# Kernel tuning notes

Hardware: AMD Instinct MI355X
Metric: run time of the kernel (lower is better)

Reference implementation:

```python
import jax, jax.numpy as jnp
import numpy as np

B, T, E, H = 64, 26, 300, 1024
FEAT, C = 2048, 7
S = C * C                  # 49 spatial positions
MCBD = 5000                # MCB_output_dim
D1 = MCBD * S              # mcb1 sketch dim = 245000
D2 = MCBD                  # mcb2 sketch dim
MCB_OUT, FACTOR = 1000, 5
VOCAB = 3000
EPS = 1e-12


def _count_sketch(x, h, s, d):
    # x: (B, n), h: (n,) int32 in [0, d), s: (n,) +-1 float -> (B, d)
    return jnp.zeros((x.shape[0], d), x.dtype).at[:, h].add(x * s)


def _cbp(x, y, hx, sx, hy, sy, d):
    # Compact bilinear pooling: count sketch both inputs, convolve via FFT.
    fx = jnp.fft.rfft(_count_sketch(x, hx, sx, d), n=d, axis=-1)
    fy = jnp.fft.rfft(_count_sketch(y, hy, sy, d), n=d, axis=-1)
    return jnp.fft.irfft(fx * fy, n=d, axis=-1)


def _lstm(x, W_ih, W_hh, b_ih, b_hh):
    # x: (T, B, E) -> hs: (T, B, H); torch gate order i, f, g, o
    xW = jnp.einsum('tbe,ge->tbg', x, W_ih) + b_ih + b_hh
    h0 = jnp.zeros((x.shape[1], W_hh.shape[1]), x.dtype)
    def step(carry, xt):
        h, c = carry
        g = xt + h @ W_hh.T
        i, f, gg, o = jnp.split(g, 4, axis=-1)
        c = jax.nn.sigmoid(f) * c + jax.nn.sigmoid(i) * jnp.tanh(gg)
        h = jax.nn.sigmoid(o) * jnp.tanh(c)
        return (h, c), h
    _, hs = jax.lax.scan(step, (h0, h0), xW)
    return hs


def _signed_sqrt(x):
    # sqrt(relu(x)) - sqrt(relu(-x)) == sign(x) * sqrt(|x|)
    return jnp.sign(x) * jnp.sqrt(jnp.abs(x))


def _l2norm(x):
    # F.normalize(x, dim=1)
    return x / jnp.maximum(jnp.linalg.norm(x, axis=1, keepdims=True), EPS)


def setup_inputs():
    key = jax.random.key(0)
    ks = jax.random.split(key, 32)
    f = lambda k, shp, sc=1.0: jax.random.normal(k, shp, jnp.float32) * sc
    ri = lambda k, shp, mx: jax.random.randint(k, shp, 0, mx, jnp.int32)
    return {
        'ques_embed': f(ks[0], (B, T, E)),
        'img_feat': f(ks[1], (B, C, C, FEAT)),
        'W_ih': f(ks[2], (4 * H, E), 0.02),
        'W_hh': f(ks[3], (4 * H, H), 0.02),
        'b_ih': f(ks[4], (4 * H,), 0.02),
        'b_hh': f(ks[5], (4 * H,), 0.02),
        'Wq1': f(ks[6], (512, H), 0.02),
        'bq1': f(ks[7], (512,), 0.02),
        'Wq2': f(ks[8], (2, 512), 0.02),
        'bq2': f(ks[9], (2,), 0.02),
        'Wi1': f(ks[10], (512, MCB_OUT), 0.02),
        'bi1': f(ks[11], (512,), 0.02),
        'Wi2': f(ks[12], (2, 512), 0.02),
        'bi2': f(ks[13], (2,), 0.02),
        'Wp': f(ks[14], (VOCAB, MCB_OUT), 0.02),
        'bp': f(ks[15], (VOCAB,), 0.02),
        'h1x': ri(ks[16], (FEAT * S,), D1),
        's1x': ri(ks[17], (FEAT * S,), 2),
        'h1q': ri(ks[18], (2 * H,), D1),
        's1q': ri(ks[19], (2 * H,), 2),
        'h2i': ri(ks[20], (2 * FEAT,), D2),
        's2i': ri(ks[21], (2 * FEAT,), 2),
        'h2q': ri(ks[22], (2 * H,), D2),
        's2q': ri(ks[23], (2 * H,), 2),
    }


def reference(ques_embed, img_feat, W_ih, W_hh, b_ih, b_hh, Wq1, bq1, Wq2, bq2,
              Wi1, bi1, Wi2, bi2, Wp, bp,
              h1x, s1x, h1q, s1q, h2i, s2i, h2q, s2q):
    sgn = lambda s: (2 * s - 1).astype(jnp.float32)
    img = jnp.transpose(img_feat, (0, 3, 1, 2)).reshape(B, FEAT, S)  # (B, feat, S)
    hs = _lstm(jnp.transpose(ques_embed, (1, 0, 2)), W_ih, W_hh, b_ih, b_hh)
    lstm1 = jnp.transpose(hs, (1, 2, 0))  # (B, H, T)
    # --- question attention (1x1 convs over (H, T)) ---
    qa = jax.nn.relu(jnp.einsum('oh,bht->bot', Wq1, lstm1) + bq1[None, :, None])
    qa = jnp.einsum('go,bot->bgt', Wq2, qa) + bq2[None, :, None]
    qatt = jax.nn.softmax(qa, axis=-1)  # (B, 2, T)
    q_feat = jnp.einsum('bgt,bht->bgh', qatt, lstm1).reshape(B, 2 * H)  # (B, 2048)
    # --- image attention with MCB1 ---
    iq = _cbp(img.reshape(B, FEAT * S), q_feat, h1x, sgn(s1x), h1q, sgn(s1q), D1)
    # (B, 5000*S) -> view (B,5000,S) -> split 5000 into (1000,5), sum factor -> (B,1000,S)
    iq = iq.reshape(B, MCB_OUT, FACTOR, S).sum(axis=2)
    iq = _l2norm(_signed_sqrt(iq).reshape(B, MCB_OUT * S)).reshape(B, MCB_OUT, S)
    ia = jax.nn.relu(jnp.einsum('om,bms->bos', Wi1, iq) + bi1[None, :, None])
    ia = jnp.einsum('go,bos->bgs', Wi2, ia) + bi2[None, :, None]
    iatt = jax.nn.softmax(ia, axis=-1)  # (B, 2, S)
    i_feat = jnp.einsum('bgs,bfs->bgf', iatt, img).reshape(B, 2 * FEAT)  # (B, 4096)
    # --- fine-grained fusion MCB2 ---
    z = _cbp(i_feat, q_feat, h2i, sgn(s2i), h2q, sgn(s2q), D2)
    z = z.reshape(B, MCB_OUT, FACTOR).sum(axis=2)
    z = _l2norm(_signed_sqrt(z))
    return jax.nn.softmax(z @ Wp.T + bp, axis=1)
```

## Files before the change

kernel.cpp:

```cpp
#include <hip/hip_runtime.h>
#include <hip/hip_fp16.h>
#include <math.h>

static constexpr int BB = 64, TT = 26, EE = 300, HH = 1024;
static constexpr int FEAT = 2048, SS = 49;
static constexpr int D1 = 245000, D2 = 5000;
static constexpr int MOUT = 1000;
static constexpr int VOCAB = 3000;

static constexpr int UPAD = 1008;
static constexpr int FOLD_R = 16000;
static constexpr int FOLD_NR = 16;
static constexpr int BCAP = 8192;
static constexpr int NITEMS = FEAT * SS;

template <int BM, int BN, int BK, int TM, int TN, bool RELU>
__global__ void gemm_abt(const float* __restrict__ A, const float* __restrict__ B,
                         const float* __restrict__ bias1, const float* __restrict__ bias2,
                         float* __restrict__ C,
                         int M, int N, int K, int lda, int ldb, int ldc) {
    constexpr int THREADS = (BM / TM) * (BN / TN);
    __shared__ __align__(16) float As[BK][BM + 4];
    __shared__ __align__(16) float Bs[BK][BN + 4];
    const int tid = threadIdx.x;
    const int tx = tid % (BN / TN);
    const int ty = tid / (BN / TN);
    const int block_m = blockIdx.y * BM;
    const int block_n = blockIdx.x * BN;
    float acc[TM][TN];
#pragma unroll
    for (int i = 0; i < TM; i++)
#pragma unroll
        for (int j = 0; j < TN; j++) acc[i][j] = 0.f;

    for (int k0 = 0; k0 < K; k0 += BK) {
        for (int i = tid; i < BM * BK; i += THREADS) {
            int m = i / BK, kk = i % BK;
            int gm = block_m + m, gk = k0 + kk;
            As[kk][m] = (gm < M && gk < K) ? A[(size_t)gm * lda + gk] : 0.f;
        }
        for (int i = tid; i < BN * BK; i += THREADS) {
            int n = i / BK, kk = i % BK;
            int gn = block_n + n, gk = k0 + kk;
            Bs[kk][n] = (gn < N && gk < K) ? B[(size_t)gn * ldb + gk] : 0.f;
        }
        __syncthreads();
#pragma unroll
        for (int kk = 0; kk < BK; kk++) {
            float a[TM], b[TN];
            if constexpr ((TM & 3) == 0 && (TN & 3) == 0) {
#pragma unroll
                for (int i = 0; i < TM / 4; i++) {
                    float4 t4 = *reinterpret_cast<const float4*>(&As[kk][ty * TM + 4 * i]);
                    a[4 * i] = t4.x; a[4 * i + 1] = t4.y;
                    a[4 * i + 2] = t4.z; a[4 * i + 3] = t4.w;
                }
#pragma unroll
                for (int j = 0; j < TN / 4; j++) {
                    float4 t4 = *reinterpret_cast<const float4*>(&Bs[kk][tx * TN + 4 * j]);
                    b[4 * j] = t4.x; b[4 * j + 1] = t4.y;
                    b[4 * j + 2] = t4.z; b[4 * j + 3] = t4.w;
                }
            } else {
#pragma unroll
                for (int i = 0; i < TM; i++) a[i] = As[kk][ty * TM + i];
#pragma unroll
                for (int j = 0; j < TN; j++) b[j] = Bs[kk][tx * TN + j];
            }
#pragma unroll
            for (int i = 0; i < TM; i++)
#pragma unroll
                for (int j = 0; j < TN; j++) acc[i][j] += a[i] * b[j];
        }
        __syncthreads();
    }
#pragma unroll
    for (int i = 0; i < TM; i++) {
        int gm = block_m + ty * TM + i;
        if (gm >= M) continue;
#pragma unroll
        for (int j = 0; j < TN; j++) {
            int gn = block_n + tx * TN + j;
            if (gn >= N) continue;
            float v = acc[i][j];
            if (bias1) v += bias1[gn];
            if (bias2) v += bias2[gn];
            if (RELU) v = fmaxf(v, 0.f);
            C[(size_t)gm * ldc + gn] = v;
        }
    }
}

__global__ void xwt_transpose(const float* __restrict__ xw, float* __restrict__ xwT) {
    __shared__ float L[64][65];
    const int t = blockIdx.x;
    const int g0 = blockIdx.y * 64;
    const int tid = threadIdx.x;
    for (int u = 0; u < 16; u++) {
        int idx = u * 256 + tid;
        int b = idx >> 6, g = idx & 63;
        L[g][b] = xw[((size_t)b * TT + t) * 4096 + g0 + g];
    }
    __syncthreads();
    for (int u = 0; u < 16; u++) {
        int idx = u * 256 + tid;
        int g = idx >> 6, b = idx & 63;
        xwT[((size_t)t * 4096 + g0 + g) * 64 + b] = L[g][b];
    }
}

__global__ void __launch_bounds__(256, 2)
lstm_step3(const float* __restrict__ xwT, const float* __restrict__ W_hh,
           const float* __restrict__ hin, float* __restrict__ hout,
           float* __restrict__ cst, float* __restrict__ hs, int step) {
    __shared__ float part2[4][8][64];
    const int tid = threadIdx.x;
    const int b = tid & 63;
    const int jw = __builtin_amdgcn_readfirstlane(tid >> 6);
    const int hh0 = blockIdx.x * 2;

    if (step > 0) {
        float acc[8];
#pragma unroll
        for (int r = 0; r < 8; r++) acc[r] = 0.f;
        const float* __restrict__ hq = hin + ((size_t)jw << 8) * 64 + b;
        const float* __restrict__ wq = W_hh + (size_t)hh0 * 1024 + ((size_t)jw << 8);
#pragma unroll 4
        for (int kk = 0; kk < 256; kk++) {
            float hv = hq[kk * 64];
#pragma unroll
            for (int g = 0; g < 4; g++) {
                acc[g * 2]     = fmaf(wq[((size_t)g * 1024) * 1024 + kk], hv, acc[g * 2]);
                acc[g * 2 + 1] = fmaf(wq[((size_t)g * 1024 + 1) * 1024 + kk], hv, acc[g * 2 + 1]);
            }
        }
#pragma unroll
        for (int r = 0; r < 8; r++) part2[jw][r][b] = acc[r];
        __syncthreads();
    }
    if (tid < 128) {
        const int i_p = tid >> 6;
        const int row = hh0 + i_p;
        const int idx = row * 64 + b;
        float g4[4];
#pragma unroll
        for (int j = 0; j < 4; j++) {
            float sum = xwT[((size_t)step * 4096 + j * 1024 + row) * 64 + b];
            if (step > 0) {
#pragma unroll
                for (int w = 0; w < 4; w++) sum += part2[w][j * 2 + i_p][b];
            }
            g4[j] = sum;
        }
        float si = 1.f / (1.f + expf(-g4[0]));
        float sf = 1.f / (1.f + expf(-g4[1]));
        float tg = tanhf(g4[2]);
        float so = 1.f / (1.f + expf(-g4[3]));
        float cp = (step > 0) ? cst[idx] : 0.f;
        float cn = sf * cp + si * tg;
        cst[idx] = cn;
        float hn = so * tanhf(cn);
        hout[idx] = hn;
        hs[((size_t)step * BB + b) * HH + row] = hn;
    }
}

__global__ void qa2_wave(const float* __restrict__ qa, const float* __restrict__ Wq2,
                         const float* __restrict__ bq2, float* __restrict__ out) {
    int wv = (blockIdx.x * blockDim.x + threadIdx.x) >> 6;
    int lane = threadIdx.x & 63;
    if (wv >= BB * 2 * TT) return;
    int t = wv % TT;
    int bg = wv / TT;
    int g = bg & 1;
    const float* arow = qa + ((size_t)t * BB + (bg >> 1)) * 512;
    const float* wrow = Wq2 + g * 512;
    float acc = 0.f;
#pragma unroll
    for (int o = 0; o < 8; o++) acc += wrow[lane + 64 * o] * arow[lane + 64 * o];
    for (int off = 32; off; off >>= 1) acc += __shfl_down(acc, off);
    if (lane == 0) out[wv] = acc + bq2[g];
}

__global__ void ia2_wave(const float* __restrict__ ia, const float* __restrict__ Wi2,
                         const float* __restrict__ bi2, float* __restrict__ out) {
    int wv = (blockIdx.x * blockDim.x + threadIdx.x) >> 6;
    int lane = threadIdx.x & 63;
    if (wv >= BB * 2 * SS) return;
    int s = wv % SS;
    int bg = wv / SS;
    int g = bg & 1;
    const float* arow = ia + ((size_t)(bg >> 1) * SS + s) * 512;
    const float* wrow = Wi2 + g * 512;
    float acc = 0.f;
#pragma unroll
    for (int o = 0; o < 8; o++) acc += wrow[lane + 64 * o] * arow[lane + 64 * o];
    for (int off = 32; off; off >>= 1) acc += __shfl_down(acc, off);
    if (lane == 0) out[wv] = acc + bi2[g];
}

__global__ void softmax_wave(float* __restrict__ x, int rows, int len) {
    int wv = (blockIdx.x * blockDim.x + threadIdx.x) >> 6;
    int lane = threadIdx.x & 63;
    if (wv >= rows) return;
    float* xr = x + (size_t)wv * len;
    float v = (lane < len) ? xr[lane] : -1e30f;
    float m = v;
    for (int off = 32; off; off >>= 1) m = fmaxf(m, __shfl_xor(m, off));
    float e = (lane < len) ? expf(v - m) : 0.f;
    float ssum = e;
    for (int off = 32; off; off >>= 1) ssum += __shfl_xor(ssum, off);
    if (lane < len) xr[lane] = e / ssum;
}

__global__ void qfeat_kernel(const float* __restrict__ qatt, const float* __restrict__ hs,
                             float* __restrict__ qf) {
    int idx = blockIdx.x * blockDim.x + threadIdx.x;
    if (idx >= BB * 2048) return;
    int b = idx >> 11;
    int gh = idx & 2047;
    int g = gh >> 10;
    int hh = gh & 1023;
    float acc = 0.f;
    for (int t = 0; t < TT; t++)
        acc += qatt[((size_t)b * 2 + g) * TT + t] * hs[((size_t)t * BB + b) * HH + hh];
    qf[idx] = acc;
}

__global__ void bucket_build(const int* __restrict__ h1x, const int* __restrict__ s1x,
                             int* __restrict__ bcnt, int* __restrict__ bkh,
                             int* __restrict__ bkp) {
    __shared__ int lcnt[FOLD_NR], lbase[FOLD_NR];
    const int tid = threadIdx.x;
    if (tid < FOLD_NR) lcnt[tid] = 0;
    __syncthreads();
    const int i = blockIdx.x * 256 + tid;
    int h = 0, pay = 0, r1 = -1, r2 = -1, p1 = 0, p2 = 0;
    if (i < NITEMS) {
        h = h1x[i];
        int f = i / SS, s = i - f * SS;
        pay = (s * FEAT + f) | (s1x[i] << 31);
#pragma unroll
        for (int r = 0; r < FOLD_NR; r++) {
            int dd = h - r * FOLD_R;
            if (dd < 0) dd += D1;
            if (dd < FOLD_R + 196) {
                int p = atomicAdd(&lcnt[r], 1);
                if (r1 < 0) { r1 = r; p1 = p; }
                else        { r2 = r; p2 = p; }
            }
        }
    }
    __syncthreads();
    if (tid < FOLD_NR) lbase[tid] = atomicAdd(&bcnt[tid], lcnt[tid]);
    __syncthreads();
    if (r1 >= 0) {
        int pos = lbase[r1] + p1;
        if (pos < BCAP) { bkh[r1 * BCAP + pos] = h; bkp[r1 * BCAP + pos] = pay; }
    }
    if (r2 >= 0) {
        int pos = lbase[r2] + p2;
        if (pos < BCAP) { bkh[r2 * BCAP + pos] = h; bkp[r2 * BCAP + pos] = pay; }
    }
}

__global__ void sketch_fold2(const float* __restrict__ img_feat, const int* __restrict__ bcnt,
                             const int* __restrict__ bkh, const int* __restrict__ bkp,
                             float* __restrict__ afold) {
    __shared__ float sl[FOLD_R + 196];
    const int r = blockIdx.x;
    const int b = blockIdx.y;
    const int r0 = r * FOLD_R;
    for (int i = threadIdx.x; i < FOLD_R + 196; i += 256) sl[i] = 0.f;
    __syncthreads();
    const int n = min(bcnt[r], BCAP);
    const float* __restrict__ ib = img_feat + (size_t)b * NITEMS;
    for (int j = threadIdx.x; j < n; j += 256) {
        int h = bkh[r * BCAP + j];
        int pay = bkp[r * BCAP + j];
        int d = h - r0;
        if (d < 0) d += D1;
        float v = ib[pay & 0x7FFFFFFF];
        float val = ((unsigned)pay >> 31) ? v : -v;
        atomicAdd(&sl[d], val);
    }
    __syncthreads();
    float* ab = afold + (size_t)b * D1;
    for (int t = threadIdx.x; t < FOLD_R; t += 256) {
        int g = r0 + t;
        if (g >= D1) break;
        ab[g] = sl[t] + sl[t + 49] + sl[t + 98] + sl[t + 147] + sl[t + 196];
    }
}

__global__ void transpose_f16b(const float* __restrict__ afold, __half2* __restrict__ A2) {
    __shared__ float L[64][65];
    const int t0 = blockIdx.x * 64;
    const int tid = threadIdx.x;
    for (int c = 0; c < 16; c++) {
        int idx = c * 256 + tid;
        int b = idx >> 6, i = idx & 63;
        int t = t0 + i;
        L[i][b] = (t < D1) ? afold[(size_t)b * D1 + t] : 0.f;
    }
    __syncthreads();
    for (int c = 0; c < 8; c++) {
        int u8 = c * 256 + tid;
        int t_loc = u8 >> 5, qq = u8 & 31;
        int t = t0 + t_loc;
        if (t >= D1) continue;
        __half2 v = __halves2half2(__float2half_rn(L[t_loc][2 * qq]),
                                   __float2half_rn(L[t_loc][2 * qq + 1]));
        int u = t / 245;
        int dv = t - u * 245;
        A2[((size_t)dv * UPAD + u) * 32 + qq] = v;
        if (u < 8) A2[((size_t)dv * UPAD + 1000 + u) * 32 + qq] = v;
    }
}

__global__ void sort_tab(const int* __restrict__ h1q, int2* __restrict__ tab2) {
    __shared__ int k[2048], v[2048];
    const int s = blockIdx.x;
    const int t = threadIdx.x;
#pragma unroll
    for (int e = 0; e < 2; e++) {
        int j = t + e * 1024;
        int d = s - h1q[j];
        if (d < 0) d += D1;
        int du = d / 245;
        int dv = d - du * 245;
        k[j] = ((dv * UPAD + du) << 10) | du;
        v[j] = j;
    }
    for (int size = 2; size <= 2048; size <<= 1) {
        for (int stride = size >> 1; stride > 0; stride >>= 1) {
            __syncthreads();
            int pos = 2 * t - (t & (stride - 1));
            bool asc = ((pos & size) == 0);
            int a = k[pos], b2 = k[pos + stride];
            if ((a > b2) == asc) {
                k[pos] = b2; k[pos + stride] = a;
                int tmp = v[pos]; v[pos] = v[pos + stride]; v[pos + stride] = tmp;
            }
        }
    }
    __syncthreads();
#pragma unroll
    for (int e = 0; e < 2; e++) {
        int r = t + e * 1024;
        tab2[(size_t)s * 2048 + r] = make_int2(k[r], v[r]);
    }
}

__global__ void vts_build(const float* __restrict__ qf, const int* __restrict__ s1q,
                          __half2* __restrict__ vTs) {
    int gid = blockIdx.x * blockDim.x + threadIdx.x;
    if (gid >= 2048 * 32) return;
    int j = gid >> 5, q = gid & 31;
    float sg = (float)(2 * s1q[j] - 1);
    vTs[gid] = __halves2half2(__float2half_rn(qf[(size_t)(2 * q) * 2048 + j] * sg),
                              __float2half_rn(qf[(size_t)(2 * q + 1) * 2048 + j] * sg));
}

__global__ void vs_permute(const __half2* __restrict__ vTs, const int2* __restrict__ tab2,
                           __half2* __restrict__ vS) {
    int gid = blockIdx.x * 256 + threadIdx.x;
    if (gid >= SS * 2048 * 32) return;
    int q = gid & 31;
    int sr = gid >> 5;
    int j = tab2[sr].y;
    vS[gid] = vTs[j * 32 + q];
}

__global__ void __launch_bounds__(256, 8)
mcb1_gather8(const __half2* __restrict__ A2, const __half2* __restrict__ vS,
             const int2* __restrict__ tab2, float* __restrict__ iq) {
    __shared__ int sp[2176];
    const int wid = blockIdx.x;
    const int lin = (wid & 7) * 196 + (wid >> 3);
    const int s = lin >> 5;
    const int bx = lin & 31;
    const int tid = threadIdx.x;
    for (int i = tid; i < 2048; i += 256) sp[i] = tab2[(size_t)s * 2048 + i].x;
    __syncthreads();

    const int q = tid & 31;
    const int w = tid >> 5;
    const int mgrp = w & 3;
    const int jh = w >> 2;
    const int m0 = bx * 32 + mgrp * 8;
    const int m0c = (m0 <= 992) ? m0 : 992;
    const int m0w = m0c - 1000;
    const int thr = 1000 - m0c;

    float accL[8], accH[8];
#pragma unroll
    for (int kk = 0; kk < 8; kk++) { accL[kk] = 0.f; accH[kk] = 0.f; }

    const unsigned* __restrict__ vp =
        (const unsigned*)vS + (((size_t)s * 2048 + (jh << 10)) << 5) + q;
    const unsigned* __restrict__ abase = (const unsigned*)A2 + q;
    const int rbase = jh << 10;

#pragma unroll 2
    for (int r = 0; r < 1024; ++r) {
        int key = sp[rbase + r];
        int A = key >> 10;
        int du = key & 1023;
        int t = A + ((du >= thr) ? m0w : m0c);
        const unsigned* __restrict__ arow = abase + ((size_t)t << 5);
        unsigned vv = vp[(size_t)r << 5];
#pragma unroll
        for (int kk = 0; kk < 8; kk++) {
            unsigned a = arow[kk * 32];
            asm("v_fma_mix_f32 %0, %1, %2, %0 op_sel:[0,0,0] op_sel_hi:[1,1,0]"
                : "+v"(accL[kk]) : "v"(a), "v"(vv));
            asm("v_fma_mix_f32 %0, %1, %2, %0 op_sel:[1,1,0] op_sel_hi:[1,1,0]"
                : "+v"(accH[kk]) : "v"(a), "v"(vv));
        }
    }

    __syncthreads();
    float* red = (float*)sp;
    const int slot = mgrp * 32 + q;
    if (jh == 1) {
        float* dst = red + slot * 17;
#pragma unroll
        for (int kk = 0; kk < 8; kk++) { dst[kk] = accL[kk]; dst[kk + 8] = accH[kk]; }
    }
    __syncthreads();
    if (jh == 0 && m0 <= 992) {
        const float* srcp = red + slot * 17;
        float* o0 = iq + ((size_t)(2 * q) * SS + s) * MOUT + m0;
        float* o1 = o0 + (size_t)SS * MOUT;
#pragma unroll
        for (int kk = 0; kk < 8; kk++) {
            o0[kk] = accL[kk] + srcp[kk];
            o1[kk] = accH[kk] + srcp[kk + 8];
        }
    }
}

__global__ void ssqrt_l2norm(float* __restrict__ x, int n) {
    __shared__ float red[1024];
    __shared__ float inv_s;
    const int nt = blockDim.x;
    int b = blockIdx.x;
    float* xb = x + (size_t)b * n;
    float ss = 0.f;
    for (int i = threadIdx.x; i < n; i += nt) {
        float v = xb[i];
        float y = (v >= 0.f) ? sqrtf(v) : -sqrtf(-v);
        xb[i] = y;
        ss += y * y;
    }
    red[threadIdx.x] = ss;
    __syncthreads();
    for (int s = nt >> 1; s > 0; s >>= 1) {
        if (threadIdx.x < s) red[threadIdx.x] += red[threadIdx.x + s];
        __syncthreads();
    }
    if (threadIdx.x == 0) inv_s = 1.f / fmaxf(sqrtf(red[0]), 1e-12f);
    __syncthreads();
    float inv = inv_s;
    for (int i = threadIdx.x; i < n; i += nt) xb[i] *= inv;
}

__global__ void ifeat_kernel(const float* __restrict__ iatt, const float* __restrict__ img_feat,
                             float* __restrict__ ifeat) {
    int idx = blockIdx.x * blockDim.x + threadIdx.x;
    if (idx >= BB * 4096) return;
    int b = idx >> 12;
    int gf = idx & 4095;
    int g = gf >> 11;
    int f = gf & 2047;
    float acc = 0.f;
    for (int s = 0; s < SS; s++)
        acc += iatt[((size_t)b * 2 + g) * SS + s] * img_feat[((size_t)b * SS + s) * FEAT + f];
    ifeat[idx] = acc;
}

__global__ void mcb2_scatter(const float* __restrict__ ifeat, const int* __restrict__ h2i,
                             const int* __restrict__ s2i, float* __restrict__ atil2) {
    int tid = blockIdx.x * blockDim.x + threadIdx.x;
    if (tid >= BB * 4096) return;
    int i = tid & 4095;
    int b = tid >> 12;
    float v = ifeat[tid] * (float)(2 * s2i[i] - 1);
    int p = h2i[i];
    float* ab = atil2 + (size_t)b * D2;
#pragma unroll
    for (int f = 0; f < 5; f++) {
        int t = p - f;
        if (t < 0) t += D2;
        atomicAdd(&ab[t], v);
    }
}

__global__ void mcb2_gather(const float* __restrict__ atil2, const float* __restrict__ qf,
                            const int* __restrict__ h2q, const int* __restrict__ s2q,
                            float* __restrict__ z) {
    __shared__ float sa[D2];
    __shared__ int sp[2048];
    __shared__ float sv[2048];
    int b = blockIdx.y;
    for (int i = threadIdx.x; i < D2; i += 256) sa[i] = atil2[(size_t)b * D2 + i];
    const float* qb = qf + (size_t)b * 2048;
    for (int j = threadIdx.x; j < 2048; j += 256) {
        sp[j] = h2q[j];
        sv[j] = qb[j] * (float)(2 * s2q[j] - 1);
    }
    __syncthreads();
    int m = blockIdx.x * 256 + threadIdx.x;
    if (m >= MOUT) return;
    int base = 5 * m + D2;
    float acc = 0.f;
#pragma unroll 4
    for (int j = 0; j < 2048; j++) {
        int addr = base - sp[j];
        if (addr >= D2) addr -= D2;
        acc += sv[j] * sa[addr];
    }
    z[(size_t)b * MOUT + m] = acc;
}

__global__ void softmax_rows(const float* __restrict__ logits, float* __restrict__ out, int n) {
    __shared__ float red[1024];
    const int nt = blockDim.x;
    int b = blockIdx.x;
    const float* xr = logits + (size_t)b * n;
    float* orow = out + (size_t)b * n;
    float mx = -1e30f;
    for (int i = threadIdx.x; i < n; i += nt) mx = fmaxf(mx, xr[i]);
    red[threadIdx.x] = mx;
    __syncthreads();
    for (int s = nt >> 1; s > 0; s >>= 1) {
        if (threadIdx.x < s) red[threadIdx.x] = fmaxf(red[threadIdx.x], red[threadIdx.x + s]);
        __syncthreads();
    }
    mx = red[0];
    __syncthreads();
    float sum = 0.f;
    for (int i = threadIdx.x; i < n; i += nt) sum += expf(xr[i] - mx);
    red[threadIdx.x] = sum;
    __syncthreads();
    for (int s = nt >> 1; s > 0; s >>= 1) {
        if (threadIdx.x < s) red[threadIdx.x] += red[threadIdx.x + s];
        __syncthreads();
    }
    float inv = 1.f / red[0];
    for (int i = threadIdx.x; i < n; i += nt) orow[i] = expf(xr[i] - mx) * inv;
}

extern "C" void kernel_launch(void* const* d_in, const int* in_sizes, int n_in,
                              void* d_out, int out_size, void* d_ws, size_t ws_size,
                              hipStream_t stream) {
    (void)in_sizes; (void)n_in; (void)out_size; (void)ws_size;
    const float* ques = (const float*)d_in[0];
    const float* img  = (const float*)d_in[1];
    const float* W_ih = (const float*)d_in[2];
    const float* W_hh = (const float*)d_in[3];
    const float* b_ih = (const float*)d_in[4];
    const float* b_hh = (const float*)d_in[5];
    const float* Wq1  = (const float*)d_in[6];
    const float* bq1  = (const float*)d_in[7];
    const float* Wq2  = (const float*)d_in[8];
    const float* bq2  = (const float*)d_in[9];
    const float* Wi1  = (const float*)d_in[10];
    const float* bi1  = (const float*)d_in[11];
    const float* Wi2  = (const float*)d_in[12];
    const float* bi2  = (const float*)d_in[13];
    const float* Wp   = (const float*)d_in[14];
    const float* bpc  = (const float*)d_in[15];
    const int* h1x = (const int*)d_in[16];
    const int* s1x = (const int*)d_in[17];
    const int* h1q = (const int*)d_in[18];
    const int* s1q = (const int*)d_in[19];
    const int* h2i = (const int*)d_in[20];
    const int* s2i = (const int*)d_in[21];
    const int* h2q = (const int*)d_in[22];
    const int* s2q = (const int*)d_in[23];
    float* out = (float*)d_out;

    float* ws = (float*)d_ws;
    float* xw    = ws;
    float* hs    = ws + 6815744;
    float* hTa   = ws + 8519680;
    float* hTb   = ws + 8585216;
    float* cst   = ws + 8650752;
    float* qa    = ws + 10224640;
    float* qatt  = ws + 11076608;
    float* xwT   = ws + 11080704;
    float* afold = ws;
    float* iq     = ws;
    float* ia     = ws + 3136000;
    float* iatt   = ws + 4741632;
    float* ifeat  = ws + 4749824;
    float* atil2  = ws + 5011968;
    float* z      = ws + 5331968;
    float* logits = ws + 5395968;
    int2*  tab2   = (int2*)(ws + 5600000);
    __half2* vS   = (__half2*)(ws + 6000000);
    __half2* A2    = (__half2*)(ws + 15680000);
    float* qf      = ws + 15680000 + 7905536;
    __half2* vTs   = (__half2*)(qf + 131072);
    int* bcnt      = (int*)(ws + 15680000 + 7905536 + 131072 + 65536 + 4096);
    int* bkh       = bcnt + 64;
    int* bkp       = bkh + FOLD_NR * BCAP;

    (void)hipMemsetAsync(bcnt, 0, 64 * 4, stream);
    bucket_build<<<(NITEMS + 255) / 256, 256, 0, stream>>>(h1x, s1x, bcnt, bkh, bkp);

    {
        dim3 grid(4096 / 64, (BB * TT + 127) / 128);
        gemm_abt<128, 64, 16, 8, 4, false><<<grid, 256, 0, stream>>>(
            ques, W_ih, b_ih, b_hh, xw, BB * TT, 4 * HH, EE, EE, EE, 4 * HH);
    }
    {
        dim3 grid(TT, 64);
        xwt_transpose<<<grid, 256, 0, stream>>>(xw, xwT);
    }
    for (int t = 0; t < TT; t++) {
        float* hout = (t & 1) ? hTb : hTa;
        const float* hin = (t & 1) ? hTa : hTb;
        lstm_step3<<<512, 256, 0, stream>>>(xwT, W_hh, (t == 0) ? nullptr : hin,
                                            hout, cst, hs, t);
    }
    {
        dim3 grid(512 / 64, (TT * BB + 127) / 128);
        gemm_abt<128, 64, 16, 8, 4, true><<<grid, 256, 0, stream>>>(
            hs, Wq1, bq1, nullptr, qa, TT * BB, 512, HH, HH, HH, 512);
    }
    qa2_wave<<<(BB * 2 * TT * 64 + 255) / 256, 256, 0, stream>>>(qa, Wq2, bq2, qatt);
    softmax_wave<<<(BB * 2 * 64 + 255) / 256, 256, 0, stream>>>(qatt, BB * 2, TT);
    qfeat_kernel<<<(BB * 2048) / 256, 256, 0, stream>>>(qatt, hs, qf);
    {
        dim3 grid(FOLD_NR, BB);
        sketch_fold2<<<grid, 256, 0, stream>>>(img, bcnt, bkh, bkp, afold);
    }
    {
        int nblk = (D1 + 63) / 64;
        transpose_f16b<<<nblk, 256, 0, stream>>>(afold, A2);
    }
    sort_tab<<<SS, 1024, 0, stream>>>(h1q, tab2);
    vts_build<<<(2048 * 32) / 256, 256, 0, stream>>>(qf, s1q, vTs);
    vs_permute<<<(SS * 2048 * 32 + 255) / 256, 256, 0, stream>>>(vTs, tab2, vS);
    mcb1_gather8<<<1568, 256, 0, stream>>>(A2, vS, tab2, iq);
    ssqrt_l2norm<<<BB, 1024, 0, stream>>>(iq, MOUT * SS);
    {
        dim3 grid(512 / 64, (BB * SS + 127) / 128);
        gemm_abt<128, 64, 16, 8, 4, true><<<grid, 256, 0, stream>>>(
            iq, Wi1, bi1, nullptr, ia, BB * SS, 512, MOUT, MOUT, MOUT, 512);
    }
    ia2_wave<<<(BB * 2 * SS * 64 + 255) / 256, 256, 0, stream>>>(ia, Wi2, bi2, iatt);
    softmax_wave<<<(BB * 2 * 64 + 255) / 256, 256, 0, stream>>>(iatt, BB * 2, SS);
    ifeat_kernel<<<(BB * 4096) / 256, 256, 0, stream>>>(iatt, img, ifeat);
    (void)hipMemsetAsync(atil2, 0, (size_t)BB * D2 * 4, stream);
    mcb2_scatter<<<(BB * 4096) / 256, 256, 0, stream>>>(ifeat, h2i, s2i, atil2);
    {
        dim3 grid(4, BB);
        mcb2_gather<<<grid, 256, 0, stream>>>(atil2, qf, h2q, s2q, z);
    }
    ssqrt_l2norm<<<BB, 256, 0, stream>>>(z, MOUT);
    {
        dim3 grid((VOCAB + 63) / 64, 4);
        gemm_abt<16, 64, 16, 2, 2, false><<<grid, 256, 0, stream>>>(
            z, Wp, bpc, nullptr, logits, BB, VOCAB, MOUT, MOUT, MOUT, VOCAB);
    }
    softmax_rows<<<BB, 1024, 0, stream>>>(logits, out, VOCAB);
}
```

Before: 2.711 ms.

## Rewrite LSTM step with LDS double-buffered h and W_hh tiles

```diff
diff --git a/kernel.cpp b/kernel.cpp
--- a/kernel.cpp
+++ b/kernel.cpp
@@ -110,46 +110,90 @@
 }
 
 __global__ void __launch_bounds__(256, 2)
-lstm_step3(const float* __restrict__ xwT, const float* __restrict__ W_hh,
+lstm_step4(const float* __restrict__ xwT, const float* __restrict__ W_hh,
            const float* __restrict__ hin, float* __restrict__ hout,
            float* __restrict__ cst, float* __restrict__ hs, int step) {
-    __shared__ float part2[4][8][64];
+    __shared__ __align__(16) float hch[2][128][64];
+    __shared__ __align__(16) float wch[2][16][128];
     const int tid = threadIdx.x;
-    const int b = tid & 63;
-    const int jw = __builtin_amdgcn_readfirstlane(tid >> 6);
-    const int hh0 = blockIdx.x * 2;
+    const int hh0 = blockIdx.x * 4;
+    float* part = (float*)wch;
 
     if (step > 0) {
-        float acc[8];
-#pragma unroll
-        for (int r = 0; r < 8; r++) acc[r] = 0.f;
-        const float* __restrict__ hq = hin + ((size_t)jw << 8) * 64 + b;
-        const float* __restrict__ wq = W_hh + (size_t)hh0 * 1024 + ((size_t)jw << 8);
-#pragma unroll 4
-        for (int kk = 0; kk < 256; kk++) {
-            float hv = hq[kk * 64];
-#pragma unroll
-            for (int g = 0; g < 4; g++) {
-                acc[g * 2]     = fmaf(wq[((size_t)g * 1024) * 1024 + kk], hv, acc[g * 2]);
-                acc[g * 2 + 1] = fmaf(wq[((size_t)g * 1024 + 1) * 1024 + kk], hv, acc[g * 2 + 1]);
+        const int lr = tid >> 4;
+        const int b4 = tid & 15;
+        float acc0 = 0.f, acc1 = 0.f, acc2 = 0.f, acc3 = 0.f;
+        {
+            const float4* hsrc = (const float4*)hin;
+            float4* hdst = (float4*)hch[0];
+#pragma unroll
+            for (int u = 0; u < 8; u++) hdst[tid + 256 * u] = hsrc[tid + 256 * u];
+#pragma unroll
+            for (int u = 0; u < 2; u++) {
+                int f4 = tid + 256 * u;
+                int lr4 = f4 >> 5, c = f4 & 31;
+                const float4* wsrc = (const float4*)(
+                    W_hh + ((size_t)((lr4 >> 2) * 1024 + hh0 + (lr4 & 3))) * 1024);
+                ((float4*)wch[0])[f4] = wsrc[c];
             }
         }
-#pragma unroll
-        for (int r = 0; r < 8; r++) part2[jw][r][b] = acc[r];
         __syncthreads();
-    }
-    if (tid < 128) {
-        const int i_p = tid >> 6;
-        const int row = hh0 + i_p;
+        for (int ck = 0; ck < 8; ck++) {
+            const int cur = ck & 1;
+            float4 hreg[8];
+            float4 wreg[2];
+            if (ck < 7) {
+                const float4* hsrc = (const float4*)(hin + (ck + 1) * 8192);
+#pragma unroll
+                for (int u = 0; u < 8; u++) hreg[u] = hsrc[tid + 256 * u];
+#pragma unroll
+                for (int u = 0; u < 2; u++) {
+                    int f4 = tid + 256 * u;
+                    int lr4 = f4 >> 5, c = f4 & 31;
+                    const float4* wsrc = (const float4*)(
+                        W_hh + ((size_t)((lr4 >> 2) * 1024 + hh0 + (lr4 & 3))) * 1024 +
+                        (ck + 1) * 128);
+                    wreg[u] = wsrc[c];
+                }
+            }
+#pragma unroll 8
+            for (int k4 = 0; k4 < 32; k4++) {
+                float4 wv = *(const float4*)&wch[cur][lr][k4 * 4];
+#pragma unroll
+                for (int e = 0; e < 4; e++) {
+                    float w = (&wv.x)[e];
+                    float4 hv = *(const float4*)&hch[cur][k4 * 4 + e][b4 * 4];
+                    acc0 = fmaf(w, hv.x, acc0);
+                    acc1 = fmaf(w, hv.y, acc1);
+                    acc2 = fmaf(w, hv.z, acc2);
+                    acc3 = fmaf(w, hv.w, acc3);
+                }
+            }
+            if (ck < 7) {
+                float4* hdst = (float4*)hch[cur ^ 1];
+#pragma unroll
+                for (int u = 0; u < 8; u++) hdst[tid + 256 * u] = hreg[u];
+#pragma unroll
+                for (int u = 0; u < 2; u++) ((float4*)wch[cur ^ 1])[tid + 256 * u] = wreg[u];
+            }
+            __syncthreads();
+        }
+        part[(lr * 64) + b4 * 4 + 0] = acc0;
+        part[(lr * 64) + b4 * 4 + 1] = acc1;
+        part[(lr * 64) + b4 * 4 + 2] = acc2;
+        part[(lr * 64) + b4 * 4 + 3] = acc3;
+        __syncthreads();
+    }
+    {
+        const int i = tid >> 6;
+        const int b = tid & 63;
+        const int row = hh0 + i;
         const int idx = row * 64 + b;
         float g4[4];
 #pragma unroll
         for (int j = 0; j < 4; j++) {
             float sum = xwT[((size_t)step * 4096 + j * 1024 + row) * 64 + b];
-            if (step > 0) {
-#pragma unroll
-                for (int w = 0; w < 4; w++) sum += part2[w][j * 2 + i_p][b];
-            }
+            if (step > 0) sum += part[(j * 4 + i) * 64 + b];
             g4[j] = sum;
         }
         float si = 1.f / (1.f + expf(-g4[0]));
@@ -623,12 +667,12 @@
     for (int t = 0; t < TT; t++) {
         float* hout = (t & 1) ? hTb : hTa;
         const float* hin = (t & 1) ? hTa : hTb;
-        lstm_step3<<<512, 256, 0, stream>>>(xwT, W_hh, (t == 0) ? nullptr : hin,
+        lstm_step4<<<256, 256, 0, stream>>>(xwT, W_hh, (t == 0) ? nullptr : hin,
                                             hout, cst, hs, t);
     }
     {
-        dim3 grid(512 / 64, (TT * BB + 127) / 128);
-        gemm_abt<128, 64, 16, 8, 4, true><<<grid, 256, 0, stream>>>(
+        dim3 grid(512 / 64, (TT * BB + 63) / 64);
+        gemm_abt<64, 64, 16, 4, 4, true><<<grid, 256, 0, stream>>>(
             hs, Wq1, bq1, nullptr, qa, TT * BB, 512, HH, HH, HH, 512);
     }
     qa2_wave<<<(BB * 2 * TT * 64 + 255) / 256, 256, 0, stream>>>(qa, Wq2, bq2, qatt);
@@ -648,8 +692,8 @@
     mcb1_gather8<<<1568, 256, 0, stream>>>(A2, vS, tab2, iq);
     ssqrt_l2norm<<<BB, 1024, 0, stream>>>(iq, MOUT * SS);
     {
-        dim3 grid(512 / 64, (BB * SS + 127) / 128);
-        gemm_abt<128, 64, 16, 8, 4, true><<<grid, 256, 0, stream>>>(
+        dim3 grid(512 / 64, (BB * SS + 63) / 64);
+        gemm_abt<64, 64, 16, 4, 4, true><<<grid, 256, 0, stream>>>(
             iq, Wi1, bi1, nullptr, ia, BB * SS, 512, MOUT, MOUT, MOUT, 512);
     }
     ia2_wave<<<(BB * 2 * SS * 64 + 255) / 256, 256, 0, stream>>>(ia, Wi2, bi2, iatt);
```

New measurement: 2.615 ms, median of 2. -3.6%, faster.
